# Performance work log

Measured on AMD Instinct MI355X. Metric: run time of the kernel, lower is better.

Reference implementation:

```python
import jax, jax.numpy as jnp
import numpy as np

N_ATOMS = 131072
N_ELEM = 4
D_IN = 128
D_HID = 256
D_OUT = 1


def setup_inputs() -> dict:
    key = jax.random.key(0)
    k1, k2, k3, k4, k5, k6 = jax.random.split(key, 6)
    descriptors = jax.random.normal(k1, (N_ATOMS, D_IN), dtype=jnp.float32)
    element_ids = jax.random.randint(k2, (N_ATOMS,), 0, N_ELEM, dtype=jnp.int32)
    # per-element 2-layer MLP params, stacked over the element (expert) axis
    s1 = 1.0 / np.sqrt(D_IN)
    s2 = 1.0 / np.sqrt(D_HID)
    W1 = jax.random.uniform(k3, (N_ELEM, D_IN, D_HID), minval=-s1, maxval=s1, dtype=jnp.float32)
    b1 = jax.random.uniform(k4, (N_ELEM, D_HID), minval=-s1, maxval=s1, dtype=jnp.float32)
    W2 = jax.random.uniform(k5, (N_ELEM, D_HID, D_OUT), minval=-s2, maxval=s2, dtype=jnp.float32)
    b2 = jax.random.uniform(k6, (N_ELEM, D_OUT), minval=-s2, maxval=s2, dtype=jnp.float32)
    return {"descriptors": descriptors, "element_ids": element_ids,
            "W1": W1, "b1": b1, "W2": W2, "b2": b2}


def reference(descriptors, element_ids, W1, b1, W2, b2):
    # Dense all-expert compute then per-atom select (E is tiny, avoids
    # materializing a per-atom gathered [N, D_IN, D_HID] weight tensor).
    h = jnp.tanh(jnp.einsum('ni,eih->neh', descriptors, W1) + b1[None])  # [N,E,H]
    y = jnp.einsum('neh,eho->neo', h, W2) + b2[None]                      # [N,E,O]
    idx = element_ids.astype(jnp.int32)[:, None, None]                    # [N,1,1]
    per_atom = jnp.take_along_axis(y, idx, axis=1)[:, 0, :]               # [N,O]
    total_energy = per_atom.sum(axis=0)                                   # [O]
    return total_energy
```

## Files before the change

### kernel.cpp

```cpp
#include <hip/hip_runtime.h>
#include <hip/hip_bf16.h>
#include <stdint.h>

#define N_ATOMS 131072
#define D_IN    128
#define D_HID   256
#define N_ELEM  4
#define NPAD    (N_ATOMS + N_ELEM * 64)
#define K4_BLOCKS 256
#define HIST_BLOCKS 128

typedef __attribute__((ext_vector_type(8))) short bf16x8;
typedef __attribute__((ext_vector_type(4))) float f32x4;

#define WS_BPART  262272
#define WS_BCNT   270592
#define WS_SIDX   287232

__device__ __forceinline__ unsigned short f2bf_rne(float f) {
    union { float f; unsigned u; } v; v.f = f;
    unsigned r = v.u + 0x7FFFu + ((v.u >> 16) & 1u);
    return (unsigned short)(r >> 16);
}

__device__ __forceinline__ bf16x8 cvt8(f32x4 v0, f32x4 v1) {
    uint4 o;
    o.x = (__float_as_uint(v0[0]) >> 16) | (__float_as_uint(v0[1]) & 0xFFFF0000u);
    o.y = (__float_as_uint(v0[2]) >> 16) | (__float_as_uint(v0[3]) & 0xFFFF0000u);
    o.z = (__float_as_uint(v1[0]) >> 16) | (__float_as_uint(v1[1]) & 0xFFFF0000u);
    o.w = (__float_as_uint(v1[2]) >> 16) | (__float_as_uint(v1[3]) & 0xFFFF0000u);
    return __builtin_bit_cast(bf16x8, o);
}

__device__ __forceinline__ int4 wave_reduce4(int4 v) {
    #pragma unroll
    for (int off = 32; off; off >>= 1) {
        v.x += __shfl_xor(v.x, off);
        v.y += __shfl_xor(v.y, off);
        v.z += __shfl_xor(v.z, off);
        v.w += __shfl_xor(v.w, off);
    }
    return v;
}

__global__ void tnn_k1_fused(const int* __restrict__ eid, int* __restrict__ bcnt,
                             const float* __restrict__ W1, unsigned short* __restrict__ W1t) {
    __shared__ float tile[64][65];
    __shared__ int lc[N_ELEM];
    int t = threadIdx.x;
    if (blockIdx.x < 32) {
        int b  = blockIdx.x;
        int e  = b >> 3;
        int k0 = ((b >> 2) & 1) * 64;
        int h0 = (b & 3) * 64;
        int cg = t & 15;
        int rr = t >> 4;
        const float* src = W1 + ((size_t)e * D_IN + k0) * D_HID + h0;
        #pragma unroll
        for (int j = 0; j < 4; ++j) {
            int row = rr + j * 16;
            f32x4 v = *(const f32x4*)(src + (size_t)row * D_HID + cg * 4);
            tile[row][cg * 4 + 0] = v[0];
            tile[row][cg * 4 + 1] = v[1];
            tile[row][cg * 4 + 2] = v[2];
            tile[row][cg * 4 + 3] = v[3];
        }
        __syncthreads();
        unsigned short* dst = W1t + ((size_t)e * D_HID + h0) * D_IN + k0;
        #pragma unroll
        for (int j = 0; j < 4; ++j) {
            int hrow = rr + j * 16;
            ushort4 o;
            o.x = f2bf_rne(tile[cg * 4 + 0][hrow]);
            o.y = f2bf_rne(tile[cg * 4 + 1][hrow]);
            o.z = f2bf_rne(tile[cg * 4 + 2][hrow]);
            o.w = f2bf_rne(tile[cg * 4 + 3][hrow]);
            *(ushort4*)(dst + (size_t)hrow * D_IN + cg * 4) = o;
        }
    } else {
        int hb = blockIdx.x - 32;
        if (t < N_ELEM) lc[t] = 0;
        __syncthreads();
        int base = hb * 1024;
        #pragma unroll
        for (int r = 0; r < 4; ++r)
            atomicAdd(&lc[eid[base + r * 256 + t]], 1);
        __syncthreads();
        if (t < N_ELEM) bcnt[hb * 4 + t] = lc[t];
    }
}

__global__ void tnn_k3_scatter(const int* __restrict__ eid, const int* __restrict__ bcnt,
                               int* __restrict__ sortedIdx) {
    __shared__ int lc[N_ELEM];
    __shared__ int base4[N_ELEM];
    int t = threadIdx.x;
    int b = blockIdx.x;
    if (t < N_ELEM) lc[t] = 0;
    if (t < 64) {
        int4 cl = ((const int4*)bcnt)[t];
        int4 ch = ((const int4*)bcnt)[t + 64];
        int4 tot = {cl.x + ch.x, cl.y + ch.y, cl.z + ch.z, cl.w + ch.w};
        tot = wave_reduce4(tot);
        int4 pre = {(t < b) ? cl.x : 0, (t < b) ? cl.y : 0,
                    (t < b) ? cl.z : 0, (t < b) ? cl.w : 0};
        if (t + 64 < b) { pre.x += ch.x; pre.y += ch.y; pre.z += ch.z; pre.w += ch.w; }
        pre = wave_reduce4(pre);
        if (t == 0) {
            int st0 = 0;
            int st1 = st0 + ((tot.x + 63) & ~63);
            int st2 = st1 + ((tot.y + 63) & ~63);
            int st3 = st2 + ((tot.z + 63) & ~63);
            base4[0] = st0 + pre.x;
            base4[1] = st1 + pre.y;
            base4[2] = st2 + pre.z;
            base4[3] = st3 + pre.w;
        }
    }
    __syncthreads();
    int base = b * 1024;
    #pragma unroll
    for (int r = 0; r < 4; ++r) {
        int i = base + r * 256 + t;
        int e = eid[i];
        int rank = atomicAdd(&lc[e], 1);
        sortedIdx[base4[e] + rank] = i;
    }
}

__global__ __launch_bounds__(512, 4) void tnn_k4_mlp(
        const float* __restrict__ X, const int* __restrict__ sortedIdx,
        const int* __restrict__ bcnt, const unsigned short* __restrict__ W1t,
        const float* __restrict__ b1, const float* __restrict__ W2,
        float* __restrict__ bpart) {
    __shared__ unsigned char ldsB[65536];
    __shared__ float2 ldsBW[256];
    const float C2 = 2.8853900817779268f;

    int t = threadIdx.x;
    int wid  = t >> 6;
    int lane = t & 63;
    int l15  = lane & 15;
    int lk   = lane >> 4;
    int e    = blockIdx.x & 3;
    int q    = blockIdx.x >> 2;

    int4 cl = ((const int4*)bcnt)[lane];
    int4 ch = ((const int4*)bcnt)[lane + 64];
    int4 tot = {cl.x + ch.x, cl.y + ch.y, cl.z + ch.z, cl.w + ch.w};
    tot = wave_reduce4(tot);
    int cnts[4] = {tot.x, tot.y, tot.z, tot.w};
    int st[5];
    st[0] = 0;
    #pragma unroll
    for (int i = 0; i < 4; ++i) st[i + 1] = st[i] + ((cnts[i] + 63) & ~63);
    int bstart = st[e];
    int cnt    = cnts[e];
    int rend   = bstart + cnt;
    int Te     = (st[e + 1] - bstart) >> 5;
    int fb     = (cnt > 0) ? sortedIdx[bstart] : 0;

    {
        int hrow  = t >> 1;
        int khalf = t & 1;
        const unsigned short* src = W1t + ((size_t)e * D_HID + hrow) * D_IN + khalf * 64;
        #pragma unroll
        for (int jj = 0; jj < 8; ++jj) {
            bf16x8 v = *(const bf16x8*)(src + jj * 8);
            *(bf16x8*)(ldsB + (khalf * 8 + jj) * 4096 + hrow * 16) = v;
        }
        if (t < 256) ldsBW[t] = make_float2(b1[e * D_HID + t] * C2, W2[e * D_HID + t]);
    }
    __syncthreads();

    unsigned ldso = (unsigned)lk * 4096u + (unsigned)l15 * 16u;

    float partial = 0.f;
    for (int tt = q * 8 + wid; tt < Te; tt += 512) {
        int tb = bstart + tt * 32;
        bool full = (tb + 32 <= rend);

        int slot0 = tb + l15, slot1 = slot0 + 16;
        int r0 = (slot0 < rend) ? sortedIdx[slot0] : fb;
        int r1 = (slot1 < rend) ? sortedIdx[slot1] : fb;

        bf16x8 a0[4], a1[4];
        const float* x0 = X + (size_t)r0 * D_IN + lk * 8;
        const float* x1 = X + (size_t)r1 * D_IN + lk * 8;
        #pragma unroll
        for (int ks = 0; ks < 4; ++ks)
            a0[ks] = cvt8(*(const f32x4*)(x0 + ks * 32), *(const f32x4*)(x0 + ks * 32 + 4));
        #pragma unroll
        for (int ks = 0; ks < 4; ++ks)
            a1[ks] = cvt8(*(const f32x4*)(x1 + ks * 32), *(const f32x4*)(x1 + ks * 32 + 4));

        float fnval = 8.f;
        if (!full) {
            int nv = 0;
            #pragma unroll
            for (int m = 0; m < 2; ++m)
                #pragma unroll
                for (int r = 0; r < 4; ++r)
                    nv += (tb + m * 16 + lk * 4 + r < rend) ? 1 : 0;
            fnval = (float)nv;
        }

        #pragma unroll 1
        for (int nt = 0; nt < 16; ++nt) {
            const unsigned char* lb = ldsB + ldso + (unsigned)nt * 256u;
            bf16x8 cur0 = *(const bf16x8*)(lb);
            bf16x8 cur1 = *(const bf16x8*)(lb + 16384);
            bf16x8 cur2 = *(const bf16x8*)(lb + 32768);
            bf16x8 cur3 = *(const bf16x8*)(lb + 49152);
            float2 bw = ldsBW[nt * 16 + l15];

            f32x4 acc0 = {0.f, 0.f, 0.f, 0.f};
            f32x4 acc1 = {0.f, 0.f, 0.f, 0.f};
            acc0 = __builtin_amdgcn_mfma_f32_16x16x32_bf16(a0[0], cur0, acc0, 0, 0, 0);
            acc1 = __builtin_amdgcn_mfma_f32_16x16x32_bf16(a1[0], cur0, acc1, 0, 0, 0);
            acc0 = __builtin_amdgcn_mfma_f32_16x16x32_bf16(a0[1], cur1, acc0, 0, 0, 0);
            acc1 = __builtin_amdgcn_mfma_f32_16x16x32_bf16(a1[1], cur1, acc1, 0, 0, 0);
            acc0 = __builtin_amdgcn_mfma_f32_16x16x32_bf16(a0[2], cur2, acc0, 0, 0, 0);
            acc1 = __builtin_amdgcn_mfma_f32_16x16x32_bf16(a1[2], cur2, acc1, 0, 0, 0);
            acc0 = __builtin_amdgcn_mfma_f32_16x16x32_bf16(a0[3], cur3, acc0, 0, 0, 0);
            acc1 = __builtin_amdgcn_mfma_f32_16x16x32_bf16(a1[3], cur3, acc1, 0, 0, 0);

            float rsum = 0.f;
            #pragma unroll
            for (int r = 0; r < 4; ++r) {
                float e0 = __builtin_amdgcn_exp2f(fmaf(C2, acc0[r], bw.x));
                float e1 = __builtin_amdgcn_exp2f(fmaf(C2, acc1[r], bw.x));
                float rc0 = __builtin_amdgcn_rcpf(e0 + 1.f);
                float rc1 = __builtin_amdgcn_rcpf(e1 + 1.f);
                if (!full) {
                    rc0 = (tb + lk * 4 + r      < rend) ? rc0 : 0.f;
                    rc1 = (tb + 16 + lk * 4 + r < rend) ? rc1 : 0.f;
                }
                rsum += rc0 + rc1;
            }
            partial = fmaf(bw.y, fmaf(-2.f, rsum, fnval), partial);
        }
    }

    #pragma unroll
    for (int off = 32; off; off >>= 1)
        partial += __shfl_down(partial, off);
    if (lane == 0) bpart[blockIdx.x * 8 + wid] = partial;
}

__global__ void tnn_k5_reduce(const float* __restrict__ bpart, const int* __restrict__ bcnt,
                              const float* __restrict__ b2, float* __restrict__ out) {
    __shared__ float r[4];
    int t = threadIdx.x;
    float s = 0.f;
    #pragma unroll
    for (int j = 0; j < 8; ++j) s += bpart[j * 256 + t];
    #pragma unroll
    for (int off = 32; off; off >>= 1)
        s += __shfl_down(s, off);
    if ((t & 63) == 0) r[t >> 6] = s;
    __syncthreads();
    if (t < 64) {
        int4 cl = ((const int4*)bcnt)[t];
        int4 ch = ((const int4*)bcnt)[t + 64];
        int4 tot = {cl.x + ch.x, cl.y + ch.y, cl.z + ch.z, cl.w + ch.w};
        tot = wave_reduce4(tot);
        if (t == 0) {
            float acc = r[0] + r[1] + r[2] + r[3];
            acc += (float)tot.x * b2[0];
            acc += (float)tot.y * b2[1];
            acc += (float)tot.z * b2[2];
            acc += (float)tot.w * b2[3];
            out[0] = acc;
        }
    }
}

extern "C" void kernel_launch(void* const* d_in, const int* in_sizes, int n_in,
                              void* d_out, int out_size, void* d_ws, size_t ws_size,
                              hipStream_t stream) {
    const float* X   = (const float*)d_in[0];
    const int*   eid = (const int*)  d_in[1];
    const float* W1  = (const float*)d_in[2];
    const float* b1  = (const float*)d_in[3];
    const float* W2  = (const float*)d_in[4];
    const float* b2  = (const float*)d_in[5];
    float* out = (float*)d_out;

    char* ws = (char*)d_ws;
    unsigned short* W1t = (unsigned short*)ws;
    float* bpart     = (float*)(ws + WS_BPART);
    int*   bcnt      = (int*)  (ws + WS_BCNT);
    int*   sortedIdx = (int*)  (ws + WS_SIDX);

    hipLaunchKernelGGL(tnn_k1_fused,   dim3(32 + HIST_BLOCKS), dim3(256), 0, stream, eid, bcnt, W1, W1t);
    hipLaunchKernelGGL(tnn_k3_scatter, dim3(HIST_BLOCKS),      dim3(256), 0, stream, eid, bcnt, sortedIdx);
    hipLaunchKernelGGL(tnn_k4_mlp,     dim3(K4_BLOCKS),        dim3(512), 0, stream,
                       X, sortedIdx, bcnt, W1t, b1, W2, bpart);
    hipLaunchKernelGGL(tnn_k5_reduce,  dim3(1),                dim3(256), 0, stream, bpart, bcnt, b2, out);
}
```

Baseline: 42.61 us.

## Double MLP grid, aggregate histogram atomics per wave, specialize full-tile loop

Raises the MLP kernel grid from 256 to 512 blocks, with the tile stride and reduction sized to match, so more workgroups share the per-expert tiles. The histogram and scatter kernels now use ballot masks to do one shared-memory atomic per expert per wave instead of one per thread. The inner loop is templated on whether a tile is full, removing the bounds-masking selects for full tiles. More blocks also means each block repeats the 64KB weight staging into LDS, and the workspace offset for bcnt moves to make room for the larger partial buffer.

```diff
diff --git a/kernel.cpp b/kernel.cpp
--- a/kernel.cpp
+++ b/kernel.cpp
@@ -7,14 +7,15 @@
 #define D_HID   256
 #define N_ELEM  4
 #define NPAD    (N_ATOMS + N_ELEM * 64)
-#define K4_BLOCKS 256
+#define K4_BLOCKS 512
 #define HIST_BLOCKS 128
 
 typedef __attribute__((ext_vector_type(8))) short bf16x8;
 typedef __attribute__((ext_vector_type(4))) float f32x4;
+typedef unsigned long long ull;
 
 #define WS_BPART  262272
-#define WS_BCNT   270592
+#define WS_BCNT   278784
 #define WS_SIDX   287232
 
 __device__ __forceinline__ unsigned short f2bf_rne(float f) {
@@ -41,6 +42,13 @@
         v.w += __shfl_xor(v.w, off);
     }
     return v;
+}
+
+__device__ __forceinline__ ull same_expert_mask(int e) {
+    ull m0 = __ballot(e & 1);
+    ull m1 = __ballot(e & 2);
+    ull m = (e & 1) ? m0 : ~m0;
+    return m & ((e & 2) ? m1 : ~m1);
 }
 
 __global__ void tnn_k1_fused(const int* __restrict__ eid, int* __restrict__ bcnt,
@@ -79,12 +87,17 @@
         }
     } else {
         int hb = blockIdx.x - 32;
+        int lane = t & 63;
         if (t < N_ELEM) lc[t] = 0;
         __syncthreads();
         int base = hb * 1024;
         #pragma unroll
-        for (int r = 0; r < 4; ++r)
-            atomicAdd(&lc[eid[base + r * 256 + t]], 1);
+        for (int r = 0; r < 4; ++r) {
+            int e = eid[base + r * 256 + t];
+            ull m = same_expert_mask(e);
+            if (lane == __builtin_ctzll(m))
+                atomicAdd(&lc[e], __popcll(m));
+        }
         __syncthreads();
         if (t < N_ELEM) bcnt[hb * 4 + t] = lc[t];
     }
@@ -96,6 +109,7 @@
     __shared__ int base4[N_ELEM];
     int t = threadIdx.x;
     int b = blockIdx.x;
+    int lane = t & 63;
     if (t < N_ELEM) lc[t] = 0;
     if (t < 64) {
         int4 cl = ((const int4*)bcnt)[t];
@@ -119,13 +133,63 @@
     }
     __syncthreads();
     int base = b * 1024;
+    ull below = (lane == 63) ? 0x7FFFFFFFFFFFFFFFULL : ((1ULL << lane) - 1);
     #pragma unroll
     for (int r = 0; r < 4; ++r) {
         int i = base + r * 256 + t;
         int e = eid[i];
-        int rank = atomicAdd(&lc[e], 1);
-        sortedIdx[base4[e] + rank] = i;
-    }
+        ull m = same_expert_mask(e);
+        int f = __builtin_ctzll(m);
+        int rank = __popcll(m & below);
+        int wbase = 0;
+        if (lane == f) wbase = atomicAdd(&lc[e], __popcll(m));
+        wbase = __shfl(wbase, f);
+        sortedIdx[base4[e] + wbase + rank] = i;
+    }
+}
+
+template<bool FULL>
+__device__ __forceinline__ float nt_loop(const unsigned char* ldsB, const float2* ldsBW,
+                                         unsigned ldso, const bf16x8 a0[4], const bf16x8 a1[4],
+                                         int tb, int rend, int lk, int l15, float fnval) {
+    const float C2 = 2.8853900817779268f;
+    float partial = 0.f;
+    #pragma unroll 1
+    for (int nt = 0; nt < 16; ++nt) {
+        const unsigned char* lb = ldsB + ldso + (unsigned)nt * 256u;
+        bf16x8 cur0 = *(const bf16x8*)(lb);
+        bf16x8 cur1 = *(const bf16x8*)(lb + 16384);
+        bf16x8 cur2 = *(const bf16x8*)(lb + 32768);
+        bf16x8 cur3 = *(const bf16x8*)(lb + 49152);
+        float2 bw = ldsBW[nt * 16 + l15];
+
+        f32x4 acc0 = {0.f, 0.f, 0.f, 0.f};
+        f32x4 acc1 = {0.f, 0.f, 0.f, 0.f};
+        acc0 = __builtin_amdgcn_mfma_f32_16x16x32_bf16(a0[0], cur0, acc0, 0, 0, 0);
+        acc1 = __builtin_amdgcn_mfma_f32_16x16x32_bf16(a1[0], cur0, acc1, 0, 0, 0);
+        acc0 = __builtin_amdgcn_mfma_f32_16x16x32_bf16(a0[1], cur1, acc0, 0, 0, 0);
+        acc1 = __builtin_amdgcn_mfma_f32_16x16x32_bf16(a1[1], cur1, acc1, 0, 0, 0);
+        acc0 = __builtin_amdgcn_mfma_f32_16x16x32_bf16(a0[2], cur2, acc0, 0, 0, 0);
+        acc1 = __builtin_amdgcn_mfma_f32_16x16x32_bf16(a1[2], cur2, acc1, 0, 0, 0);
+        acc0 = __builtin_amdgcn_mfma_f32_16x16x32_bf16(a0[3], cur3, acc0, 0, 0, 0);
+        acc1 = __builtin_amdgcn_mfma_f32_16x16x32_bf16(a1[3], cur3, acc1, 0, 0, 0);
+
+        float rsum = 0.f;
+        #pragma unroll
+        for (int r = 0; r < 4; ++r) {
+            float e0 = __builtin_amdgcn_exp2f(fmaf(C2, acc0[r], bw.x));
+            float e1 = __builtin_amdgcn_exp2f(fmaf(C2, acc1[r], bw.x));
+            float rc0 = __builtin_amdgcn_rcpf(e0 + 1.f);
+            float rc1 = __builtin_amdgcn_rcpf(e1 + 1.f);
+            if (!FULL) {
+                rc0 = (tb + lk * 4 + r      < rend) ? rc0 : 0.f;
+                rc1 = (tb + 16 + lk * 4 + r < rend) ? rc1 : 0.f;
+            }
+            rsum += rc0 + rc1;
+        }
+        partial = fmaf(bw.y, fmaf(-2.f, rsum, fnval), partial);
+    }
+    return partial;
 }
 
 __global__ __launch_bounds__(512, 4) void tnn_k4_mlp(
@@ -176,7 +240,7 @@
     unsigned ldso = (unsigned)lk * 4096u + (unsigned)l15 * 16u;
 
     float partial = 0.f;
-    for (int tt = q * 8 + wid; tt < Te; tt += 512) {
+    for (int tt = q * 8 + wid; tt < Te; tt += 1024) {
         int tb = bstart + tt * 32;
         bool full = (tb + 32 <= rend);
 
@@ -194,51 +258,16 @@
         for (int ks = 0; ks < 4; ++ks)
             a1[ks] = cvt8(*(const f32x4*)(x1 + ks * 32), *(const f32x4*)(x1 + ks * 32 + 4));
 
-        float fnval = 8.f;
-        if (!full) {
+        if (full) {
+            partial += nt_loop<true >(ldsB, ldsBW, ldso, a0, a1, tb, rend, lk, l15, 8.f);
+        } else {
             int nv = 0;
             #pragma unroll
             for (int m = 0; m < 2; ++m)
                 #pragma unroll
                 for (int r = 0; r < 4; ++r)
                     nv += (tb + m * 16 + lk * 4 + r < rend) ? 1 : 0;
-            fnval = (float)nv;
-        }
-
-        #pragma unroll 1
-        for (int nt = 0; nt < 16; ++nt) {
-            const unsigned char* lb = ldsB + ldso + (unsigned)nt * 256u;
-            bf16x8 cur0 = *(const bf16x8*)(lb);
-            bf16x8 cur1 = *(const bf16x8*)(lb + 16384);
-            bf16x8 cur2 = *(const bf16x8*)(lb + 32768);
-            bf16x8 cur3 = *(const bf16x8*)(lb + 49152);
-            float2 bw = ldsBW[nt * 16 + l15];
-
-            f32x4 acc0 = {0.f, 0.f, 0.f, 0.f};
-            f32x4 acc1 = {0.f, 0.f, 0.f, 0.f};
-            acc0 = __builtin_amdgcn_mfma_f32_16x16x32_bf16(a0[0], cur0, acc0, 0, 0, 0);
-            acc1 = __builtin_amdgcn_mfma_f32_16x16x32_bf16(a1[0], cur0, acc1, 0, 0, 0);
-            acc0 = __builtin_amdgcn_mfma_f32_16x16x32_bf16(a0[1], cur1, acc0, 0, 0, 0);
-            acc1 = __builtin_amdgcn_mfma_f32_16x16x32_bf16(a1[1], cur1, acc1, 0, 0, 0);
-            acc0 = __builtin_amdgcn_mfma_f32_16x16x32_bf16(a0[2], cur2, acc0, 0, 0, 0);
-            acc1 = __builtin_amdgcn_mfma_f32_16x16x32_bf16(a1[2], cur2, acc1, 0, 0, 0);
-            acc0 = __builtin_amdgcn_mfma_f32_16x16x32_bf16(a0[3], cur3, acc0, 0, 0, 0);
-            acc1 = __builtin_amdgcn_mfma_f32_16x16x32_bf16(a1[3], cur3, acc1, 0, 0, 0);
-
-            float rsum = 0.f;
-            #pragma unroll
-            for (int r = 0; r < 4; ++r) {
-                float e0 = __builtin_amdgcn_exp2f(fmaf(C2, acc0[r], bw.x));
-                float e1 = __builtin_amdgcn_exp2f(fmaf(C2, acc1[r], bw.x));
-                float rc0 = __builtin_amdgcn_rcpf(e0 + 1.f);
-                float rc1 = __builtin_amdgcn_rcpf(e1 + 1.f);
-                if (!full) {
-                    rc0 = (tb + lk * 4 + r      < rend) ? rc0 : 0.f;
-                    rc1 = (tb + 16 + lk * 4 + r < rend) ? rc1 : 0.f;
-                }
-                rsum += rc0 + rc1;
-            }
-            partial = fmaf(bw.y, fmaf(-2.f, rsum, fnval), partial);
+            partial += nt_loop<false>(ldsB, ldsBW, ldso, a0, a1, tb, rend, lk, l15, (float)nv);
         }
     }
 
@@ -254,7 +283,7 @@
     int t = threadIdx.x;
     float s = 0.f;
     #pragma unroll
-    for (int j = 0; j < 8; ++j) s += bpart[j * 256 + t];
+    for (int j = 0; j < 16; ++j) s += bpart[j * 256 + t];
     #pragma unroll
     for (int off = 32; off; off >>= 1)
         s += __shfl_down(s, off);
```

Measured after the change: 37.88 us. 11.1% less time.
